# Kernel tuning notes

Measured on AMD Instinct MI355X. Metric: run time of the kernel, lower is better.

The kernel has to match this reference:

```python
import jax, jax.numpy as jnp
import numpy as np

B, T, F, H = 2048, 16, 768, 1024  # batch(nodes), timesteps, 3*input_size, hidden_size


def setup_inputs() -> dict:
    key = jax.random.key(0)
    k1, k2, k3 = jax.random.split(key, 3)
    s_ih = 1.0 / np.sqrt(F)
    s_hh = 1.0 / np.sqrt(H)
    return {
        "x": jax.random.normal(k1, (B, T, F), dtype=jnp.float32),
        "W_ih": jax.random.normal(k2, (F, 4 * H), dtype=jnp.float32) * s_ih,
        "W_hh": jax.random.normal(k3, (H, 4 * H), dtype=jnp.float32) * s_hh,
        "b": jnp.zeros((4 * H,), dtype=jnp.float32),
    }


def reference(x, W_ih, W_hh, b):
    # Batched equivalent of the original per-sample python loop:
    # each sample's [T, F] sequence runs through the LSTM; the final hidden
    # state [H] per sample is concatenated and reshaped to (-1, B).
    Bb, Tt, Ff = x.shape
    Hh = W_hh.shape[0]
    x_t = jnp.swapaxes(x, 0, 1)  # [T, B, F]

    def step(carry, xt):
        h, c = carry
        gates = xt @ W_ih + h @ W_hh + b  # [B, 4H]
        i, f, g, o = jnp.split(gates, 4, axis=-1)
        c = jax.nn.sigmoid(f) * c + jax.nn.sigmoid(i) * jnp.tanh(g)
        h = jax.nn.sigmoid(o) * jnp.tanh(c)
        return (h, c), None

    h0 = jnp.zeros((Bb, Hh), dtype=x.dtype)
    (h, _), _ = jax.lax.scan(step, (h0, h0), x_t)
    # torch.cat over batch of [H] vectors -> flat [B*H], then reshape(-1, B)
    return h.reshape(-1).reshape(-1, Bb)
```

## Files before the change

### kernel.cpp

```cpp
#include <hip/hip_runtime.h>
#include <hip/hip_bf16.h>
#include <stdint.h>

#define B_  2048
#define T_  16
#define F_  768
#define H_  1024
#define G4_ 4096

typedef __attribute__((ext_vector_type(8))) __bf16 bf16x8;
typedef __attribute__((ext_vector_type(4))) float  f32x4;

static __device__ __forceinline__ unsigned short f2bf(float f) {
    union { float f; uint32_t u; } v; v.f = f;
    uint32_t u = v.u;
    uint32_t r = (u + 0x7fffu + ((u >> 16) & 1u)) >> 16;
    return (unsigned short)r;
}
static __device__ __forceinline__ unsigned short f2h(float f) {
    union { _Float16 h; unsigned short u; } v; v.h = (_Float16)f; return v.u;
}
static __device__ __forceinline__ float h2f(unsigned short u) {
    union { _Float16 h; unsigned short u; } v; v.u = u; return (float)v.h;
}
static __device__ __forceinline__ float sigf(float x) {
    return 1.0f / (1.0f + __expf(-x));
}
static __device__ __forceinline__ float tanhfast(float x) {
    return 2.0f / (1.0f + __expf(-2.0f * x)) - 1.0f;
}

#define GLOAD_LDS16(gsrc, ldst)                                                       \
    __builtin_amdgcn_global_load_lds((const __attribute__((address_space(1))) void*)(gsrc), \
                                     (__attribute__((address_space(3))) void*)(ldst), \
                                     16, 0, 0)


__global__ void convert_x_kernel(const float* __restrict__ x,
                                 unsigned short* __restrict__ xbf, int n4) {
    int idx = blockIdx.x * blockDim.x + threadIdx.x;
    if (idx >= n4) return;
    float4 v = *(const float4*)(x + (size_t)idx * 4);
    ushort4 o;
    o.x = f2bf(v.x); o.y = f2bf(v.y); o.z = f2bf(v.z); o.w = f2bf(v.w);
    *(ushort4*)(xbf + (size_t)idx * 4) = o;
}

__global__ void transpose_w_kernel(const float* __restrict__ w,
                                   unsigned short* __restrict__ wt, int K) {
    __shared__ float tile[32][33];
    int nb = blockIdx.x * 32;
    int kb = blockIdx.y * 32;
    int tx = threadIdx.x, ty = threadIdx.y;
    #pragma unroll
    for (int i = 0; i < 32; i += 8)
        tile[ty + i][tx] = w[(size_t)(kb + ty + i) * G4_ + nb + tx];
    __syncthreads();
    #pragma unroll
    for (int i = 0; i < 32; i += 8) {
        int n = nb + ty + i;
        int g = n >> 10;
        int j = n & 1023;
        int np = (j >> 6) * 256 + g * 64 + ((j >> 4) & 3) * 16 + (j & 15);
        wt[(size_t)np * K + kb + tx] = f2bf(tile[tx][ty + i]);
    }
}


#define STAGE_A(slot, kt) do {                                                        \
    const int kel_ = (kt) * 64;                                                       \
    _Pragma("unroll")                                                                 \
    for (int r2 = 0; r2 < 2; ++r2) {                                                  \
        const int rih_ = r2 * 64 + (tid >> 3);                                        \
        const int ch_  = (tid & 7) ^ (rih_ & 7);                                      \
        GLOAD_LDS16(SRC_A + (size_t)(bm0 + rih_) * LD_A + kel_ + ch_ * 8,             \
                    &ldsA[slot][r2 * 4096 + tid * 8]);                                \
    }                                                                                 \
} while (0)

#define STAGE_B(bufi, half, kt) do {                                                  \
    const int kel_ = (kt) * 64;                                                       \
    _Pragma("unroll")                                                                 \
    for (int r2 = 0; r2 < 2; ++r2) {                                                  \
        const int rih_ = r2 * 64 + (tid >> 3);                                        \
        const int ch_  = (tid & 7) ^ (rih_ & 7);                                      \
        GLOAD_LDS16(SRC_B + (size_t)(bn0 + (half) * 128 + rih_) * LD_B + kel_ + ch_ * 8, \
                    &ldsB[bufi][half][r2 * 4096 + tid * 8]);                          \
    }                                                                                 \
} while (0)

#define RD_A2(slot, AR, mlo)                                                          \
    _Pragma("unroll")                                                                 \
    for (int m2 = 0; m2 < 2; ++m2) {                                                  \
        const int row_ = wm * 64 + ((mlo) + m2) * 16 + fr;                            \
        _Pragma("unroll")                                                             \
        for (int kk = 0; kk < 2; ++kk)                                                \
            AR[m2][kk] = *(const bf16x8*)&ldsA[slot]                                  \
                [row_ * 64 + (((kk * 4 + fq) ^ (row_ & 7)) * 8)];                     \
    }

#define RD_B4(bufi)                                                                   \
    _Pragma("unroll")                                                                 \
    for (int nf = 0; nf < 4; ++nf) {                                                  \
        const int rih_ = (nf & 1) * 64 + wn * 16 + fr;                                \
        _Pragma("unroll")                                                             \
        for (int kk = 0; kk < 2; ++kk)                                                \
            Bf[nf][kk] = *(const bf16x8*)&ldsB[bufi][nf >> 1]                         \
                [rih_ * 64 + (((kk * 4 + fq) ^ (rih_ & 7)) * 8)];                     \
    }

#define MFMA16(AR, mb)                                                                \
    __builtin_amdgcn_s_setprio(1);                                                    \
    _Pragma("unroll")                                                                 \
    for (int mm = 0; mm < 2; ++mm)                                                    \
        _Pragma("unroll")                                                             \
        for (int nf = 0; nf < 4; ++nf)                                                \
            _Pragma("unroll")                                                         \
            for (int kk = 0; kk < 2; ++kk)                                            \
                acc[(mb) + mm][nf] = __builtin_amdgcn_mfma_f32_16x16x32_bf16(         \
                    AR[mm][kk], Bf[nf][kk], acc[(mb) + mm][nf], 0, 0, 0);             \
    __builtin_amdgcn_s_setprio(0);

#define WAIT6 asm volatile("s_waitcnt vmcnt(6)" ::: "memory");
#define LGKM0 asm volatile("s_waitcnt lgkmcnt(0)" ::: "memory");                      \
              __builtin_amdgcn_sched_barrier(0);
#define BARR  __builtin_amdgcn_s_barrier();

#define KTILE(KT, NT) do {                                                            \
    const int buf_ = (KT) & 1;                                                        \
    const int sA_  = (KT) % 3;                                                        \
    const int sA2_ = ((KT) + 2) % 3;                                                  \
    const int k2_  = ((KT) + 2 < (NT)) ? (KT) + 2 : (NT) - 1;                         \
    bf16x8 Am[2][2], Bf[4][2];                                                        \
                                                                             \
    RD_A2(sA_, Am, 0);                                                                \
    RD_B4(buf_);                                                                      \
    STAGE_A(sA2_, k2_);                                                               \
    BARR; LGKM0;                                                                      \
    MFMA16(Am, 0);                                                                    \
    BARR;                                                                             \
                                                                             \
    RD_A2(sA_, Am, 2);                                                                \
    STAGE_B(buf_, 0, k2_);                                                            \
    STAGE_B(buf_, 1, k2_);                                                            \
    WAIT6; BARR; LGKM0;                                                               \
    MFMA16(Am, 2);                                                                    \
    BARR;                                                                             \
} while (0)

#define KPROLOGUE()                                                                   \
    STAGE_A(0, 0); STAGE_B(0, 0, 0); STAGE_B(0, 1, 0);                                \
    STAGE_A(1, 1); STAGE_B(1, 0, 1); STAGE_B(1, 1, 1);                                \
    WAIT6; BARR;


__global__ __launch_bounds__(512, 1) void xgemm2_kernel(
        const unsigned short* __restrict__ xbf,
        const unsigned short* __restrict__ wih_t,
        unsigned short* __restrict__ gx) {
    __shared__ __align__(16) unsigned short ldsA[3][8192];
    __shared__ __align__(16) unsigned short ldsB[2][2][8192];

    const int bid = blockIdx.x;
    const int xcd = bid & 7;
    const int i   = bid >> 3;
    const int bn  = xcd * 2 + (i & 1);
    const int bm  = i >> 1;
    const int bm0 = bm * 128, bn0 = bn * 256;

    const int tid = threadIdx.x;
    const int wid = tid >> 6, lane = tid & 63;
    const int wm = wid >> 2, wn = wid & 3;
    const int fr = lane & 15, fq = lane >> 4;

    const unsigned short* __restrict__ SRC_A = xbf;   const int LD_A = F_;
    const unsigned short* __restrict__ SRC_B = wih_t; const int LD_B = F_;

    f32x4 acc[4][4] = {};

    KPROLOGUE();
    for (int kt = 0; kt < 12; ++kt) KTILE(kt, 12);

    const int j = bn * 64 + wn * 16 + fr;
    #pragma unroll
    for (int mm = 0; mm < 4; ++mm) {
        #pragma unroll
        for (int rr = 0; rr < 4; ++rr) {
            int row = bm0 + wm * 64 + mm * 16 + fq * 4 + rr;
            int tt = row & 15, bb = row >> 4;
            ushort4 o;
            o.x = f2h(acc[mm][0][rr]);
            o.y = f2h(acc[mm][1][rr]);
            o.z = f2h(acc[mm][2][rr]);
            o.w = f2h(acc[mm][3][rr]);
            *(ushort4*)(gx + (((size_t)tt * B_ + bb) * H_ + j) * 4) = o;
        }
    }
}


__global__ __launch_bounds__(512, 1) void lstm_step2_kernel(
        const unsigned short* __restrict__ hprev,
        const unsigned short* __restrict__ whh_t,
        const unsigned short* __restrict__ gx,
        const float* __restrict__ bias,
        float* __restrict__ c,
        unsigned short* __restrict__ hnext,
        float* __restrict__ hout,
        int t, int last) {
    __shared__ __align__(16) unsigned short ldsA[3][8192];
    __shared__ __align__(16) unsigned short ldsB[2][2][8192];

    const int bid = blockIdx.x;
    const int xcd = bid & 7;
    const int i   = bid >> 3;
    const int bn  = (xcd >> 1) * 4 + (i & 3);
    const int bm  = (xcd & 1) * 8 + (i >> 2);
    const int bm0 = bm * 128, bn0 = bn * 256;

    const int tid = threadIdx.x;
    const int wid = tid >> 6, lane = tid & 63;
    const int wm = wid >> 2, wn = wid & 3;
    const int fr = lane & 15, fq = lane >> 4;

    const unsigned short* __restrict__ SRC_A = hprev; const int LD_A = H_;
    const unsigned short* __restrict__ SRC_B = whh_t; const int LD_B = H_;

    f32x4 acc[4][4] = {};

    KPROLOGUE();
    for (int kt = 0; kt < 16; ++kt) KTILE(kt, 16);

    const int j = bn * 64 + wn * 16 + fr;
    const float b_i = bias[j];
    const float b_f = bias[H_ + j];
    const float b_g = bias[2 * H_ + j];
    const float b_o = bias[3 * H_ + j];

    #pragma unroll
    for (int mm = 0; mm < 4; ++mm) {
        #pragma unroll
        for (int rr = 0; rr < 4; ++rr) {
            int row = bm0 + wm * 64 + mm * 16 + fq * 4 + rr;
            ushort4 g4 = *(const ushort4*)(gx + (((size_t)t * B_ + row) * H_ + j) * 4);
            float gi = acc[mm][0][rr] + b_i + h2f(g4.x);
            float gf = acc[mm][1][rr] + b_f + h2f(g4.y);
            float gg = acc[mm][2][rr] + b_g + h2f(g4.z);
            float go = acc[mm][3][rr] + b_o + h2f(g4.w);
            size_t off = (size_t)row * H_ + j;
            float cold = c[off];
            float cn = sigf(gf) * cold + sigf(gi) * tanhfast(gg);
            float hv = sigf(go) * tanhfast(cn);
            c[off] = cn;
            hnext[off] = f2bf(hv);
            if (last) hout[off] = hv;
        }
    }
}


__global__ void cell0_kernel(const unsigned short* __restrict__ gx,
                             const float* __restrict__ bias,
                             float* __restrict__ c,
                             unsigned short* __restrict__ hbf) {
    int idx = blockIdx.x * blockDim.x + threadIdx.x;
    int b = idx >> 10;
    int j = idx & 1023;
    ushort4 g4 = *(const ushort4*)(gx + ((size_t)b * H_ + j) * 4);
    float gi = bias[j]          + h2f(g4.x);
    float gg = bias[2 * H_ + j] + h2f(g4.z);
    float go = bias[3 * H_ + j] + h2f(g4.w);
    float cn = sigf(gi) * tanhfast(gg);
    float hv = sigf(go) * tanhfast(cn);
    size_t off = (size_t)b * H_ + j;
    c[off] = cn;
    hbf[off] = f2bf(hv);
}


extern "C" void kernel_launch(void* const* d_in, const int* in_sizes, int n_in,
                              void* d_out, int out_size, void* d_ws, size_t ws_size,
                              hipStream_t stream) {
    const float* x    = (const float*)d_in[0];
    const float* Wih  = (const float*)d_in[1];
    const float* Whh  = (const float*)d_in[2];
    const float* bias = (const float*)d_in[3];
    float* out = (float*)d_out;

    char* ws = (char*)d_ws;
    unsigned short* xbf   = (unsigned short*)(ws);
    unsigned short* wih_t = (unsigned short*)(ws + 50331648);
    unsigned short* whh_t = (unsigned short*)(ws + 56623104);
    unsigned short* hbf0  = (unsigned short*)(ws + 65011712);
    unsigned short* hbf1  = (unsigned short*)(ws + 69206016);
    float*          c     = (float*)(ws + 73400320);
    unsigned short* gx    = (unsigned short*)(ws + 81788928);

    int n4 = B_ * T_ * F_ / 4;
    hipLaunchKernelGGL(convert_x_kernel, dim3((n4 + 255) / 256), dim3(256), 0, stream,
                       x, xbf, n4);
    hipLaunchKernelGGL(transpose_w_kernel, dim3(G4_ / 32, F_ / 32), dim3(32, 8), 0, stream,
                       Wih, wih_t, F_);
    hipLaunchKernelGGL(transpose_w_kernel, dim3(G4_ / 32, H_ / 32), dim3(32, 8), 0, stream,
                       Whh, whh_t, H_);

    hipLaunchKernelGGL(xgemm2_kernel, dim3(4096), dim3(512), 0, stream,
                       xbf, wih_t, gx);

    hipLaunchKernelGGL(cell0_kernel, dim3(B_ * H_ / 256), dim3(256), 0, stream,
                       gx, bias, c, hbf0);

    for (int t = 1; t < T_; ++t) {
        unsigned short* hr = (t & 1) ? hbf0 : hbf1;
        unsigned short* hw = (t & 1) ? hbf1 : hbf0;
        hipLaunchKernelGGL(lstm_step2_kernel, dim3(256), dim3(512), 0, stream,
                           hr, whh_t, gx, bias, c, hw, out, t, (t == T_ - 1) ? 1 : 0);
    }
}
```

Baseline: 815.5 us.

## Fuse LSTM timesteps into persistent cooperative kernel and enlarge input-GEMM tiles

Replaces the 15 per-timestep kernel launches and the separate cell0 kernel with one cooperative persistent kernel. It keeps the cell state in registers, prefetches the gx gates before each step's GEMM, and uses grid-wide syncs between steps. The input-projection GEMM moves to 256x256 tiles with a new four-phase LDS pipeline and two blocks per CU. The goal is to cut launch overhead, remove the global memory traffic for c, and raise reuse in the x GEMM. The costs are grid-sync latency and higher register and LDS pressure.

```diff
diff --git a/kernel.cpp b/kernel.cpp
--- a/kernel.cpp
+++ b/kernel.cpp
@@ -1,5 +1,6 @@
 #include <hip/hip_runtime.h>
 #include <hip/hip_bf16.h>
+#include <hip/hip_cooperative_groups.h>
 #include <stdint.h>
 
 #define B_  2048
@@ -67,126 +68,120 @@
 }
 
 
-#define STAGE_A(slot, kt) do {                                                        \
+#define STAGE4(bufi, kind, half, gbase, ld, rowbase, kt) do {                         \
     const int kel_ = (kt) * 64;                                                       \
     _Pragma("unroll")                                                                 \
     for (int r2 = 0; r2 < 2; ++r2) {                                                  \
         const int rih_ = r2 * 64 + (tid >> 3);                                        \
         const int ch_  = (tid & 7) ^ (rih_ & 7);                                      \
-        GLOAD_LDS16(SRC_A + (size_t)(bm0 + rih_) * LD_A + kel_ + ch_ * 8,             \
-                    &ldsA[slot][r2 * 4096 + tid * 8]);                                \
+        GLOAD_LDS16((gbase) + (size_t)((rowbase) + (half) * 128 + rih_) * (ld)        \
+                            + kel_ + ch_ * 8,                                         \
+                    &lds[bufi][kind][half][r2 * 4096 + tid * 8]);                     \
     }                                                                                 \
 } while (0)
 
-#define STAGE_B(bufi, half, kt) do {                                                  \
-    const int kel_ = (kt) * 64;                                                       \
-    _Pragma("unroll")                                                                 \
-    for (int r2 = 0; r2 < 2; ++r2) {                                                  \
-        const int rih_ = r2 * 64 + (tid >> 3);                                        \
-        const int ch_  = (tid & 7) ^ (rih_ & 7);                                      \
-        GLOAD_LDS16(SRC_B + (size_t)(bn0 + (half) * 128 + rih_) * LD_B + kel_ + ch_ * 8, \
-                    &ldsB[bufi][half][r2 * 4096 + tid * 8]);                          \
-    }                                                                                 \
-} while (0)
-
-#define RD_A2(slot, AR, mlo)                                                          \
-    _Pragma("unroll")                                                                 \
-    for (int m2 = 0; m2 < 2; ++m2) {                                                  \
-        const int row_ = wm * 64 + ((mlo) + m2) * 16 + fr;                            \
+#define RD4_A(half_, mb)                                                              \
+    _Pragma("unroll")                                                                 \
+    for (int mm = 0; mm < 4; ++mm) {                                                  \
+        const int row_ = ((mb) + mm) * 32 + wm * 16 + fr;                             \
         _Pragma("unroll")                                                             \
         for (int kk = 0; kk < 2; ++kk)                                                \
-            AR[m2][kk] = *(const bf16x8*)&ldsA[slot]                                  \
-                [row_ * 64 + (((kk * 4 + fq) ^ (row_ & 7)) * 8)];                     \
-    }
-
-#define RD_B4(bufi)                                                                   \
-    _Pragma("unroll")                                                                 \
-    for (int nf = 0; nf < 4; ++nf) {                                                  \
-        const int rih_ = (nf & 1) * 64 + wn * 16 + fr;                                \
+            Afr[mm][kk] = *(const bf16x8*)&lds[buf][0][half_]                         \
+                [(row_ & 127) * 64 + (((kk * 4 + fq) ^ (row_ & 7)) * 8)];             \
+    }
+
+#define RD4_B(half_, nb)                                                              \
+    _Pragma("unroll")                                                                 \
+    for (int nn = 0; nn < 2; ++nn) {                                                  \
+        const int row_ = ((nb) + nn) * 64 + wn * 16 + fr;                             \
         _Pragma("unroll")                                                             \
         for (int kk = 0; kk < 2; ++kk)                                                \
-            Bf[nf][kk] = *(const bf16x8*)&ldsB[bufi][nf >> 1]                         \
-                [rih_ * 64 + (((kk * 4 + fq) ^ (rih_ & 7)) * 8)];                     \
-    }
-
-#define MFMA16(AR, mb)                                                                \
+            Bfr[(nb) + nn][kk] = *(const bf16x8*)&lds[buf][1][half_]                  \
+                [(row_ & 127) * 64 + (((kk * 4 + fq) ^ (row_ & 7)) * 8)];             \
+    }
+
+#define MFMAQ(mb, nb)                                                                 \
     __builtin_amdgcn_s_setprio(1);                                                    \
     _Pragma("unroll")                                                                 \
-    for (int mm = 0; mm < 2; ++mm)                                                    \
-        _Pragma("unroll")                                                             \
-        for (int nf = 0; nf < 4; ++nf)                                                \
+    for (int mm = 0; mm < 4; ++mm)                                                    \
+        _Pragma("unroll")                                                             \
+        for (int nn = 0; nn < 2; ++nn)                                                \
             _Pragma("unroll")                                                         \
             for (int kk = 0; kk < 2; ++kk)                                            \
-                acc[(mb) + mm][nf] = __builtin_amdgcn_mfma_f32_16x16x32_bf16(         \
-                    AR[mm][kk], Bf[nf][kk], acc[(mb) + mm][nf], 0, 0, 0);             \
+                acc[(mb) + mm][(nb) + nn] = __builtin_amdgcn_mfma_f32_16x16x32_bf16(  \
+                    Afr[mm][kk], Bfr[(nb) + nn][kk], acc[(mb) + mm][(nb) + nn], 0, 0, 0); \
     __builtin_amdgcn_s_setprio(0);
 
-#define WAIT6 asm volatile("s_waitcnt vmcnt(6)" ::: "memory");
-#define LGKM0 asm volatile("s_waitcnt lgkmcnt(0)" ::: "memory");                      \
-              __builtin_amdgcn_sched_barrier(0);
-#define BARR  __builtin_amdgcn_s_barrier();
-
-#define KTILE(KT, NT) do {                                                            \
-    const int buf_ = (KT) & 1;                                                        \
-    const int sA_  = (KT) % 3;                                                        \
-    const int sA2_ = ((KT) + 2) % 3;                                                  \
-    const int k2_  = ((KT) + 2 < (NT)) ? (KT) + 2 : (NT) - 1;                         \
-    bf16x8 Am[2][2], Bf[4][2];                                                        \
-                                                                             \
-    RD_A2(sA_, Am, 0);                                                                \
-    RD_B4(buf_);                                                                      \
-    STAGE_A(sA2_, k2_);                                                               \
-    BARR; LGKM0;                                                                      \
-    MFMA16(Am, 0);                                                                    \
-    BARR;                                                                             \
-                                                                             \
-    RD_A2(sA_, Am, 2);                                                                \
-    STAGE_B(buf_, 0, k2_);                                                            \
-    STAGE_B(buf_, 1, k2_);                                                            \
-    WAIT6; BARR; LGKM0;                                                               \
-    MFMA16(Am, 2);                                                                    \
-    BARR;                                                                             \
-} while (0)
-
-#define KPROLOGUE()                                                                   \
-    STAGE_A(0, 0); STAGE_B(0, 0, 0); STAGE_B(0, 1, 0);                                \
-    STAGE_A(1, 1); STAGE_B(1, 0, 1); STAGE_B(1, 1, 1);                                \
-    WAIT6; BARR;
-
-
-__global__ __launch_bounds__(512, 1) void xgemm2_kernel(
+#define WAITV4  asm volatile("s_waitcnt vmcnt(10)" ::: "memory");                     \
+                __builtin_amdgcn_sched_barrier(0);
+#define BARR4   __builtin_amdgcn_s_barrier();                                         \
+                __builtin_amdgcn_sched_barrier(0);
+
+#define KLOOP4(ABASE, ALD, BBASE, BLD, NT)                                            \
+    STAGE4(0, 0, 0, ABASE, ALD, bm0, 0);                                              \
+    STAGE4(0, 1, 0, BBASE, BLD, bn0, 0);                                              \
+    STAGE4(0, 1, 1, BBASE, BLD, bn0, 0);                                              \
+    STAGE4(0, 0, 1, ABASE, ALD, bm0, 0);                                              \
+    STAGE4(1, 0, 0, ABASE, ALD, bm0, 1);                                              \
+    STAGE4(1, 1, 0, BBASE, BLD, bn0, 1);                                              \
+    STAGE4(1, 1, 1, BBASE, BLD, bn0, 1);                                              \
+    WAITV4; BARR4;                                                                    \
+    for (int kt = 0; kt < (NT); ++kt) {                                               \
+        const int buf = kt & 1, nbuf = buf ^ 1;                                       \
+        const int k1 = (kt + 1 < (NT)) ? kt + 1 : (NT) - 1;                           \
+        const int k2 = (kt + 2 < (NT)) ? kt + 2 : (NT) - 1;                           \
+        bf16x8 Afr[4][2]; bf16x8 Bfr[4][2];                                           \
+                                                                             \
+        RD4_A(0, 0); RD4_B(0, 0);                                                     \
+        STAGE4(nbuf, 0, 1, ABASE, ALD, bm0, k1);                                      \
+        WAITV4; BARR4;                                                                \
+        MFMAQ(0, 0); BARR4;                                                           \
+                                                                             \
+        RD4_B(1, 2);                                                                  \
+        STAGE4(buf, 0, 0, ABASE, ALD, bm0, k2);                                       \
+        WAITV4; BARR4;                                                                \
+        MFMAQ(0, 2); BARR4;                                                           \
+                                                                             \
+        RD4_A(1, 4);                                                                  \
+        STAGE4(buf, 1, 0, BBASE, BLD, bn0, k2);                                       \
+        BARR4;                                                                        \
+        MFMAQ(4, 0); BARR4;                                                           \
+                                                                             \
+        STAGE4(buf, 1, 1, BBASE, BLD, bn0, k2);                                       \
+        WAITV4; BARR4;                                                                \
+        MFMAQ(4, 2); BARR4;                                                           \
+    }
+
+__global__ __launch_bounds__(512, 2) void xgemm8_kernel(
         const unsigned short* __restrict__ xbf,
         const unsigned short* __restrict__ wih_t,
         unsigned short* __restrict__ gx) {
-    __shared__ __align__(16) unsigned short ldsA[3][8192];
-    __shared__ __align__(16) unsigned short ldsB[2][2][8192];
+    __shared__ __align__(16) unsigned short lds[2][2][2][8192];
 
     const int bid = blockIdx.x;
     const int xcd = bid & 7;
     const int i   = bid >> 3;
-    const int bn  = xcd * 2 + (i & 1);
-    const int bm  = i >> 1;
-    const int bm0 = bm * 128, bn0 = bn * 256;
+    const int bmg = i >> 6;
+    const int r   = i & 63;
+    const int bn  = r >> 2;
+    const int bm  = xcd * 16 + bmg * 4 + (r & 3);
+    const int bm0 = bm * 256, bn0 = bn * 256;
 
     const int tid = threadIdx.x;
     const int wid = tid >> 6, lane = tid & 63;
     const int wm = wid >> 2, wn = wid & 3;
     const int fr = lane & 15, fq = lane >> 4;
 
-    const unsigned short* __restrict__ SRC_A = xbf;   const int LD_A = F_;
-    const unsigned short* __restrict__ SRC_B = wih_t; const int LD_B = F_;
-
-    f32x4 acc[4][4] = {};
-
-    KPROLOGUE();
-    for (int kt = 0; kt < 12; ++kt) KTILE(kt, 12);
+    f32x4 acc[8][4] = {};
+
+    KLOOP4(xbf, F_, wih_t, F_, 12)
 
     const int j = bn * 64 + wn * 16 + fr;
     #pragma unroll
-    for (int mm = 0; mm < 4; ++mm) {
+    for (int mm = 0; mm < 8; ++mm) {
         #pragma unroll
         for (int rr = 0; rr < 4; ++rr) {
-            int row = bm0 + wm * 64 + mm * 16 + fq * 4 + rr;
+            int row = bm0 + mm * 32 + wm * 16 + fq * 4 + rr;
             int tt = row & 15, bb = row >> 4;
             ushort4 o;
             o.x = f2h(acc[mm][0][rr]);
@@ -199,15 +194,100 @@
 }
 
 
-__global__ __launch_bounds__(512, 1) void lstm_step2_kernel(
-        const unsigned short* __restrict__ hprev,
+#define STAGE_A(slot, kt) do {                                                        \
+    const int kel_ = (kt) * 64;                                                       \
+    _Pragma("unroll")                                                                 \
+    for (int r2 = 0; r2 < 2; ++r2) {                                                  \
+        const int rih_ = r2 * 64 + (tid >> 3);                                        \
+        const int ch_  = (tid & 7) ^ (rih_ & 7);                                      \
+        GLOAD_LDS16(SRC_A + (size_t)(bm0 + rih_) * LD_A + kel_ + ch_ * 8,             \
+                    &ldsA[slot][r2 * 4096 + tid * 8]);                                \
+    }                                                                                 \
+} while (0)
+
+#define STAGE_B(bufi, half, kt) do {                                                  \
+    const int kel_ = (kt) * 64;                                                       \
+    _Pragma("unroll")                                                                 \
+    for (int r2 = 0; r2 < 2; ++r2) {                                                  \
+        const int rih_ = r2 * 64 + (tid >> 3);                                        \
+        const int ch_  = (tid & 7) ^ (rih_ & 7);                                      \
+        GLOAD_LDS16(SRC_B + (size_t)(bn0 + (half) * 128 + rih_) * LD_B + kel_ + ch_ * 8, \
+                    &ldsB[bufi][half][r2 * 4096 + tid * 8]);                          \
+    }                                                                                 \
+} while (0)
+
+#define RD_A2(slot, AR, mlo)                                                          \
+    _Pragma("unroll")                                                                 \
+    for (int m2 = 0; m2 < 2; ++m2) {                                                  \
+        const int row_ = wm * 64 + ((mlo) + m2) * 16 + fr;                            \
+        _Pragma("unroll")                                                             \
+        for (int kk = 0; kk < 2; ++kk)                                                \
+            AR[m2][kk] = *(const bf16x8*)&ldsA[slot]                                  \
+                [row_ * 64 + (((kk * 4 + fq) ^ (row_ & 7)) * 8)];                     \
+    }
+
+#define RD_B4(bufi)                                                                   \
+    _Pragma("unroll")                                                                 \
+    for (int nf = 0; nf < 4; ++nf) {                                                  \
+        const int rih_ = (nf & 1) * 64 + wn * 16 + fr;                                \
+        _Pragma("unroll")                                                             \
+        for (int kk = 0; kk < 2; ++kk)                                                \
+            Bf[nf][kk] = *(const bf16x8*)&ldsB[bufi][nf >> 1]                         \
+                [rih_ * 64 + (((kk * 4 + fq) ^ (rih_ & 7)) * 8)];                     \
+    }
+
+#define MFMA16(AR, mb)                                                                \
+    __builtin_amdgcn_s_setprio(1);                                                    \
+    _Pragma("unroll")                                                                 \
+    for (int mm = 0; mm < 2; ++mm)                                                    \
+        _Pragma("unroll")                                                             \
+        for (int nf = 0; nf < 4; ++nf)                                                \
+            _Pragma("unroll")                                                         \
+            for (int kk = 0; kk < 2; ++kk)                                            \
+                acc[(mb) + mm][nf] = __builtin_amdgcn_mfma_f32_16x16x32_bf16(         \
+                    AR[mm][kk], Bf[nf][kk], acc[(mb) + mm][nf], 0, 0, 0);             \
+    __builtin_amdgcn_s_setprio(0);
+
+#define WAIT6 asm volatile("s_waitcnt vmcnt(6)" ::: "memory");
+#define WAIT0 asm volatile("s_waitcnt vmcnt(0)" ::: "memory");
+#define LGKM0 asm volatile("s_waitcnt lgkmcnt(0)" ::: "memory");                      \
+              __builtin_amdgcn_sched_barrier(0);
+#define BARR6 __builtin_amdgcn_s_barrier();
+
+#define KTILE(KT, NT) do {                                                            \
+    const int buf_ = (KT) & 1;                                                        \
+    const int sA_  = (KT) % 3;                                                        \
+    const int sA2_ = ((KT) + 2) % 3;                                                  \
+    const int k2_  = ((KT) + 2 < (NT)) ? (KT) + 2 : (NT) - 1;                         \
+    bf16x8 Am[2][2], Bf[4][2];                                                        \
+                                                                             \
+    RD_A2(sA_, Am, 0);                                                                \
+    RD_B4(buf_);                                                                      \
+    STAGE_A(sA2_, k2_);                                                               \
+    BARR6; LGKM0;                                                                     \
+    MFMA16(Am, 0);                                                                    \
+    BARR6;                                                                            \
+                                                                             \
+    RD_A2(sA_, Am, 2);                                                                \
+    STAGE_B(buf_, 0, k2_);                                                            \
+    STAGE_B(buf_, 1, k2_);                                                            \
+    WAIT6; BARR6; LGKM0;                                                              \
+    MFMA16(Am, 2);                                                                    \
+    BARR6;                                                                            \
+} while (0)
+
+#define KPRO6()                                                                       \
+    STAGE_A(0, 0); STAGE_B(0, 0, 0); STAGE_B(0, 1, 0);                                \
+    STAGE_A(1, 1); STAGE_B(1, 0, 1); STAGE_B(1, 1, 1);                                \
+    WAIT6; BARR6;
+
+__global__ __launch_bounds__(512, 1) void lstm_persist_kernel(
         const unsigned short* __restrict__ whh_t,
         const unsigned short* __restrict__ gx,
         const float* __restrict__ bias,
-        float* __restrict__ c,
-        unsigned short* __restrict__ hnext,
-        float* __restrict__ hout,
-        int t, int last) {
+        unsigned short* __restrict__ hb0,
+        unsigned short* __restrict__ hb1,
+        float* __restrict__ hout) {
     __shared__ __align__(16) unsigned short ldsA[3][8192];
     __shared__ __align__(16) unsigned short ldsB[2][2][8192];
 
@@ -223,13 +303,8 @@
     const int wm = wid >> 2, wn = wid & 3;
     const int fr = lane & 15, fq = lane >> 4;
 
-    const unsigned short* __restrict__ SRC_A = hprev; const int LD_A = H_;
-    const unsigned short* __restrict__ SRC_B = whh_t; const int LD_B = H_;
-
-    f32x4 acc[4][4] = {};
-
-    KPROLOGUE();
-    for (int kt = 0; kt < 16; ++kt) KTILE(kt, 16);
+    const unsigned short* __restrict__ SRC_B = whh_t;
+    const int LD_B = H_;
 
     const int j = bn * 64 + wn * 16 + fr;
     const float b_i = bias[j];
@@ -237,44 +312,71 @@
     const float b_g = bias[2 * H_ + j];
     const float b_o = bias[3 * H_ + j];
 
+    float c_reg[4][4];
+
     #pragma unroll
     for (int mm = 0; mm < 4; ++mm) {
         #pragma unroll
         for (int rr = 0; rr < 4; ++rr) {
             int row = bm0 + wm * 64 + mm * 16 + fq * 4 + rr;
-            ushort4 g4 = *(const ushort4*)(gx + (((size_t)t * B_ + row) * H_ + j) * 4);
-            float gi = acc[mm][0][rr] + b_i + h2f(g4.x);
-            float gf = acc[mm][1][rr] + b_f + h2f(g4.y);
-            float gg = acc[mm][2][rr] + b_g + h2f(g4.z);
-            float go = acc[mm][3][rr] + b_o + h2f(g4.w);
-            size_t off = (size_t)row * H_ + j;
-            float cold = c[off];
-            float cn = sigf(gf) * cold + sigf(gi) * tanhfast(gg);
+            ushort4 g4 = *(const ushort4*)(gx + ((size_t)row * H_ + j) * 4);
+            float gi = b_i + h2f(g4.x);
+            float gg = b_g + h2f(g4.z);
+            float go = b_o + h2f(g4.w);
+            float cn = sigf(gi) * tanhfast(gg);
             float hv = sigf(go) * tanhfast(cn);
-            c[off] = cn;
-            hnext[off] = f2bf(hv);
-            if (last) hout[off] = hv;
+            c_reg[mm][rr] = cn;
+            hb0[(size_t)row * H_ + j] = f2bf(hv);
         }
     }
-}
-
-
-__global__ void cell0_kernel(const unsigned short* __restrict__ gx,
-                             const float* __restrict__ bias,
-                             float* __restrict__ c,
-                             unsigned short* __restrict__ hbf) {
-    int idx = blockIdx.x * blockDim.x + threadIdx.x;
-    int b = idx >> 10;
-    int j = idx & 1023;
-    ushort4 g4 = *(const ushort4*)(gx + ((size_t)b * H_ + j) * 4);
-    float gi = bias[j]          + h2f(g4.x);
-    float gg = bias[2 * H_ + j] + h2f(g4.z);
-    float go = bias[3 * H_ + j] + h2f(g4.w);
-    float cn = sigf(gi) * tanhfast(gg);
-    float hv = sigf(go) * tanhfast(cn);
-    size_t off = (size_t)b * H_ + j;
-    c[off] = cn;
-    hbf[off] = f2bf(hv);
+    cooperative_groups::this_grid().sync();
+
+    for (int t = 1; t < T_; ++t) {
+        const unsigned short* __restrict__ SRC_A = (t & 1) ? hb0 : hb1;
+        unsigned short* __restrict__ hw = (t & 1) ? hb1 : hb0;
+        const int LD_A = H_;
+
+        ushort4 gpre[4][4];
+        #pragma unroll
+        for (int mm = 0; mm < 4; ++mm)
+            #pragma unroll
+            for (int rr = 0; rr < 4; ++rr) {
+                int row = bm0 + wm * 64 + mm * 16 + fq * 4 + rr;
+                gpre[mm][rr] = *(const ushort4*)(gx + (((size_t)t * B_ + row) * H_ + j) * 4);
+            }
+
+        f32x4 acc[4][4];
+        #pragma unroll
+        for (int mm = 0; mm < 4; ++mm)
+            #pragma unroll
+            for (int nf = 0; nf < 4; ++nf)
+                #pragma unroll
+                for (int q = 0; q < 4; ++q) acc[mm][nf][q] = 0.0f;
+
+        KPRO6();
+        for (int kt = 0; kt < 16; ++kt) KTILE(kt, 16);
+        WAIT0;
+
+        #pragma unroll
+        for (int mm = 0; mm < 4; ++mm) {
+            #pragma unroll
+            for (int rr = 0; rr < 4; ++rr) {
+                int row = bm0 + wm * 64 + mm * 16 + fq * 4 + rr;
+                ushort4 g4 = gpre[mm][rr];
+                float gi = acc[mm][0][rr] + b_i + h2f(g4.x);
+                float gf = acc[mm][1][rr] + b_f + h2f(g4.y);
+                float gg = acc[mm][2][rr] + b_g + h2f(g4.z);
+                float go = acc[mm][3][rr] + b_o + h2f(g4.w);
+                float cn = sigf(gf) * c_reg[mm][rr] + sigf(gi) * tanhfast(gg);
+                float hv = sigf(go) * tanhfast(cn);
+                c_reg[mm][rr] = cn;
+                size_t off = (size_t)row * H_ + j;
+                hw[off] = f2bf(hv);
+                if (t == T_ - 1) hout[off] = hv;
+            }
+        }
+        cooperative_groups::this_grid().sync();
+    }
 }
 
 
@@ -293,8 +395,7 @@
     unsigned short* whh_t = (unsigned short*)(ws + 56623104);
     unsigned short* hbf0  = (unsigned short*)(ws + 65011712);
     unsigned short* hbf1  = (unsigned short*)(ws + 69206016);
-    float*          c     = (float*)(ws + 73400320);
-    unsigned short* gx    = (unsigned short*)(ws + 81788928);
+    unsigned short* gx    = (unsigned short*)(ws + 73400320);
 
     int n4 = B_ * T_ * F_ / 4;
     hipLaunchKernelGGL(convert_x_kernel, dim3((n4 + 255) / 256), dim3(256), 0, stream,
@@ -304,16 +405,19 @@
     hipLaunchKernelGGL(transpose_w_kernel, dim3(G4_ / 32, H_ / 32), dim3(32, 8), 0, stream,
                        Whh, whh_t, H_);
 
-    hipLaunchKernelGGL(xgemm2_kernel, dim3(4096), dim3(512), 0, stream,
+    hipLaunchKernelGGL(xgemm8_kernel, dim3(2048), dim3(512), 0, stream,
                        xbf, wih_t, gx);
 
-    hipLaunchKernelGGL(cell0_kernel, dim3(B_ * H_ / 256), dim3(256), 0, stream,
-                       gx, bias, c, hbf0);
-
-    for (int t = 1; t < T_; ++t) {
-        unsigned short* hr = (t & 1) ? hbf0 : hbf1;
-        unsigned short* hw = (t & 1) ? hbf1 : hbf0;
-        hipLaunchKernelGGL(lstm_step2_kernel, dim3(256), dim3(512), 0, stream,
-                           hr, whh_t, gx, bias, c, hw, out, t, (t == T_ - 1) ? 1 : 0);
-    }
-}
+    {
+        const unsigned short* whh_p = whh_t;
+        const unsigned short* gx_p  = gx;
+        const float* bias_p = bias;
+        unsigned short* h0_p = hbf0;
+        unsigned short* h1_p = hbf1;
+        float* out_p = out;
+        void* kargs[6] = { (void*)&whh_p, (void*)&gx_p, (void*)&bias_p,
+                           (void*)&h0_p, (void*)&h1_p, (void*)&out_p };
+        hipLaunchCooperativeKernel((void*)lstm_persist_kernel, dim3(256), dim3(512),
+                                   kargs, 0, stream);
+    }
+}
```

Result: slower. 1.135 ms (+39.2%).

## Replace split two-phase K-tile schedule with single-barrier triple-buffered pipeline

Applied to the files above, without the earlier changes.

Each K tile was processed as two half-MFMA phases with four barriers and a double-buffered B tile. It is now processed as one phase: all A and B fragments are read at once, the next-next tile of both A and B is staged into a triple-buffered slot, one MFMA block of 32 instructions is issued, and there is a single barrier per tile. The goal is to cut barrier and synchronisation overhead and let loads overlap a longer stretch of MFMA work. In exchange, LDS use grows by one more B buffer (about 144KB total), more fragment registers are live, and the sched_barrier that pinned instruction order is removed.

```diff
diff --git a/kernel.cpp b/kernel.cpp
--- a/kernel.cpp
+++ b/kernel.cpp
@@ -78,88 +78,80 @@
     }                                                                                 \
 } while (0)
 
-#define STAGE_B(bufi, half, kt) do {                                                  \
+#define STAGE_B(slot, half, kt) do {                                                  \
     const int kel_ = (kt) * 64;                                                       \
     _Pragma("unroll")                                                                 \
     for (int r2 = 0; r2 < 2; ++r2) {                                                  \
         const int rih_ = r2 * 64 + (tid >> 3);                                        \
         const int ch_  = (tid & 7) ^ (rih_ & 7);                                      \
         GLOAD_LDS16(SRC_B + (size_t)(bn0 + (half) * 128 + rih_) * LD_B + kel_ + ch_ * 8, \
-                    &ldsB[bufi][half][r2 * 4096 + tid * 8]);                          \
+                    &ldsB[slot][half][r2 * 4096 + tid * 8]);                          \
     }                                                                                 \
 } while (0)
 
-#define RD_A2(slot, AR, mlo)                                                          \
-    _Pragma("unroll")                                                                 \
-    for (int m2 = 0; m2 < 2; ++m2) {                                                  \
-        const int row_ = wm * 64 + ((mlo) + m2) * 16 + fr;                            \
+#define RD_A4(slot, AR)                                                               \
+    _Pragma("unroll")                                                                 \
+    for (int mm = 0; mm < 4; ++mm) {                                                  \
+        const int row_ = wm * 64 + mm * 16 + fr;                                      \
         _Pragma("unroll")                                                             \
         for (int kk = 0; kk < 2; ++kk)                                                \
-            AR[m2][kk] = *(const bf16x8*)&ldsA[slot]                                  \
+            AR[mm][kk] = *(const bf16x8*)&ldsA[slot]                                  \
                 [row_ * 64 + (((kk * 4 + fq) ^ (row_ & 7)) * 8)];                     \
     }
 
-#define RD_B4(bufi)                                                                   \
+#define RD_B4(slot, BF)                                                               \
     _Pragma("unroll")                                                                 \
     for (int nf = 0; nf < 4; ++nf) {                                                  \
         const int rih_ = (nf & 1) * 64 + wn * 16 + fr;                                \
         _Pragma("unroll")                                                             \
         for (int kk = 0; kk < 2; ++kk)                                                \
-            Bf[nf][kk] = *(const bf16x8*)&ldsB[bufi][nf >> 1]                         \
+            BF[nf][kk] = *(const bf16x8*)&ldsB[slot][nf >> 1]                         \
                 [rih_ * 64 + (((kk * 4 + fq) ^ (rih_ & 7)) * 8)];                     \
     }
 
-#define MFMA16(AR, mb)                                                                \
+#define MFMA32(AR, BF)                                                                \
     __builtin_amdgcn_s_setprio(1);                                                    \
     _Pragma("unroll")                                                                 \
-    for (int mm = 0; mm < 2; ++mm)                                                    \
+    for (int mm = 0; mm < 4; ++mm)                                                    \
         _Pragma("unroll")                                                             \
         for (int nf = 0; nf < 4; ++nf)                                                \
             _Pragma("unroll")                                                         \
             for (int kk = 0; kk < 2; ++kk)                                            \
-                acc[(mb) + mm][nf] = __builtin_amdgcn_mfma_f32_16x16x32_bf16(         \
-                    AR[mm][kk], Bf[nf][kk], acc[(mb) + mm][nf], 0, 0, 0);             \
+                acc[mm][nf] = __builtin_amdgcn_mfma_f32_16x16x32_bf16(                \
+                    AR[mm][kk], BF[nf][kk], acc[mm][nf], 0, 0, 0);                    \
     __builtin_amdgcn_s_setprio(0);
 
 #define WAIT6 asm volatile("s_waitcnt vmcnt(6)" ::: "memory");
-#define LGKM0 asm volatile("s_waitcnt lgkmcnt(0)" ::: "memory");                      \
-              __builtin_amdgcn_sched_barrier(0);
+#define LGKM0 asm volatile("s_waitcnt lgkmcnt(0)" ::: "memory");
 #define BARR  __builtin_amdgcn_s_barrier();
 
-#define KTILE(KT, NT) do {                                                            \
-    const int buf_ = (KT) & 1;                                                        \
-    const int sA_  = (KT) % 3;                                                        \
-    const int sA2_ = ((KT) + 2) % 3;                                                  \
-    const int k2_  = ((KT) + 2 < (NT)) ? (KT) + 2 : (NT) - 1;                         \
-    bf16x8 Am[2][2], Bf[4][2];                                                        \
-                                                                             \
-    RD_A2(sA_, Am, 0);                                                                \
-    RD_B4(buf_);                                                                      \
-    STAGE_A(sA2_, k2_);                                                               \
-    BARR; LGKM0;                                                                      \
-    MFMA16(Am, 0);                                                                    \
-    BARR;                                                                             \
-                                                                             \
-    RD_A2(sA_, Am, 2);                                                                \
-    STAGE_B(buf_, 0, k2_);                                                            \
-    STAGE_B(buf_, 1, k2_);                                                            \
-    WAIT6; BARR; LGKM0;                                                               \
-    MFMA16(Am, 2);                                                                    \
-    BARR;                                                                             \
+#define KTILE1(KT, NT) do {                                                           \
+    const int s_  = (KT) % 3;                                                         \
+    const int s2_ = ((KT) + 2) % 3;                                                   \
+    const int k2_ = ((KT) + 2 < (NT)) ? (KT) + 2 : (NT) - 1;                          \
+    bf16x8 Am[4][2], Bf[4][2];                                                        \
+    RD_A4(s_, Am);                                                                    \
+    RD_B4(s_, Bf);                                                                    \
+    STAGE_A(s2_, k2_);                                                                \
+    STAGE_B(s2_, 0, k2_);                                                             \
+    STAGE_B(s2_, 1, k2_);                                                             \
+    LGKM0;                                                                            \
+    MFMA32(Am, Bf);                                                                   \
+    WAIT6; BARR;                                                                      \
 } while (0)
 
-#define KPROLOGUE()                                                                   \
+#define KPRO1()                                                                       \
     STAGE_A(0, 0); STAGE_B(0, 0, 0); STAGE_B(0, 1, 0);                                \
     STAGE_A(1, 1); STAGE_B(1, 0, 1); STAGE_B(1, 1, 1);                                \
     WAIT6; BARR;
 
 
-__global__ __launch_bounds__(512, 1) void xgemm2_kernel(
+__global__ __launch_bounds__(512, 1) void xgemm1_kernel(
         const unsigned short* __restrict__ xbf,
         const unsigned short* __restrict__ wih_t,
         unsigned short* __restrict__ gx) {
     __shared__ __align__(16) unsigned short ldsA[3][8192];
-    __shared__ __align__(16) unsigned short ldsB[2][2][8192];
+    __shared__ __align__(16) unsigned short ldsB[3][2][8192];
 
     const int bid = blockIdx.x;
     const int xcd = bid & 7;
@@ -178,8 +170,8 @@
 
     f32x4 acc[4][4] = {};
 
-    KPROLOGUE();
-    for (int kt = 0; kt < 12; ++kt) KTILE(kt, 12);
+    KPRO1();
+    for (int kt = 0; kt < 12; ++kt) KTILE1(kt, 12);
 
     const int j = bn * 64 + wn * 16 + fr;
     #pragma unroll
@@ -199,7 +191,7 @@
 }
 
 
-__global__ __launch_bounds__(512, 1) void lstm_step2_kernel(
+__global__ __launch_bounds__(512, 1) void lstm_step1_kernel(
         const unsigned short* __restrict__ hprev,
         const unsigned short* __restrict__ whh_t,
         const unsigned short* __restrict__ gx,
@@ -209,7 +201,7 @@
         float* __restrict__ hout,
         int t, int last) {
     __shared__ __align__(16) unsigned short ldsA[3][8192];
-    __shared__ __align__(16) unsigned short ldsB[2][2][8192];
+    __shared__ __align__(16) unsigned short ldsB[3][2][8192];
 
     const int bid = blockIdx.x;
     const int xcd = bid & 7;
@@ -228,8 +220,8 @@
 
     f32x4 acc[4][4] = {};
 
-    KPROLOGUE();
-    for (int kt = 0; kt < 16; ++kt) KTILE(kt, 16);
+    KPRO1();
+    for (int kt = 0; kt < 16; ++kt) KTILE1(kt, 16);
 
     const int j = bn * 64 + wn * 16 + fr;
     const float b_i = bias[j];
@@ -304,7 +296,7 @@
     hipLaunchKernelGGL(transpose_w_kernel, dim3(G4_ / 32, H_ / 32), dim3(32, 8), 0, stream,
                        Whh, whh_t, H_);
 
-    hipLaunchKernelGGL(xgemm2_kernel, dim3(4096), dim3(512), 0, stream,
+    hipLaunchKernelGGL(xgemm1_kernel, dim3(4096), dim3(512), 0, stream,
                        xbf, wih_t, gx);
 
     hipLaunchKernelGGL(cell0_kernel, dim3(B_ * H_ / 256), dim3(256), 0, stream,
@@ -313,7 +305,7 @@
     for (int t = 1; t < T_; ++t) {
         unsigned short* hr = (t & 1) ? hbf0 : hbf1;
         unsigned short* hw = (t & 1) ? hbf1 : hbf0;
-        hipLaunchKernelGGL(lstm_step2_kernel, dim3(256), dim3(512), 0, stream,
+        hipLaunchKernelGGL(lstm_step1_kernel, dim3(256), dim3(512), 0, stream,
                            hr, whh_t, gx, bias, c, hw, out, t, (t == T_ - 1) ? 1 : 0);
     }
 }
```

Result: faster. 777.7 us (-4.6%).
